# Optimization experiments

Hardware: AMD Instinct MI355X
Metric: run time of the kernel (lower is better)

Reference implementation:

```python
import jax, jax.numpy as jnp
import numpy as np

N, S, SKV, K, V = 16, 4096, 4096, 64, 64


def setup_inputs() -> dict:
    key = jax.random.key(0)
    k1, k2, k3, k4 = jax.random.split(key, 4)
    return {
        "queries": jax.random.normal(k1, (N, S, K), dtype=jnp.float32),
        "keys": jax.random.normal(k2, (N, SKV, K), dtype=jnp.float32),
        "values": jax.random.normal(k3, (N, SKV, V), dtype=jnp.float32),
        "mask": jax.random.normal(k4, (S, SKV), dtype=jnp.float32),
    }


def reference(queries, keys, values, mask):
    # queries scaled by K^{-1/2}, then baddbmm(mask, q, k^T)
    scale = queries.shape[-1] ** -0.5
    q = queries * scale
    # scores: [N, S, SKV]; mask (S, SKV) broadcasts over batch like baddbmm
    scores = jnp.einsum('nsk,ntk->nst', q, keys) + mask
    attn_weights = jax.nn.softmax(scores, axis=-1)
    # attn: [N, S, V]; dropout_p = 0.0 (eval), needs_weights = False
    attn = jnp.einsum('nst,ntv->nsv', attn_weights, values)
    return attn
```

## Files before the change

### kernel.cpp

```cpp
#include <hip/hip_runtime.h>
#include <cstdint>
#include <cstddef>


typedef __attribute__((ext_vector_type(8))) short short8;
typedef __attribute__((ext_vector_type(4))) short short4v;
typedef __attribute__((ext_vector_type(4))) float f32x4;
typedef __attribute__((ext_vector_type(4))) unsigned int uint4v;
typedef __attribute__((ext_vector_type(2))) unsigned int uint2v;

#define DEV __device__ __forceinline__

constexpr int N_B   = 16;
constexpr int S_Q   = 4096;
constexpr int S_KV  = 4096;
constexpr int DH    = 64;
constexpr int BQ    = 128;
constexpr int BK    = 64;
constexpr int ITERS = S_KV / BK;
constexpr int KSTR  = 72;
constexpr int VSTR  = 68;

#define LOG2E 1.44269504088896340736f
#define QSCALE (0.125f * 1.44269504088896340736f)

DEV unsigned short f2bf(float f) {
  union { float f; unsigned int i; } x; x.f = f;
  unsigned int r = x.i + 0x7FFFu + ((x.i >> 16) & 1u);
  return (unsigned short)(r >> 16);
}

#if __has_builtin(__builtin_amdgcn_cvt_pk_bf16_f32)
typedef __attribute__((ext_vector_type(2))) __bf16 bf16x2v;
DEV unsigned int packrne(float a, float b) {
  union { bf16x2v v; unsigned int u; } x;
  x.v = __builtin_amdgcn_cvt_pk_bf16_f32(a, b);
  return x.u;
}
#else
DEV unsigned int packrne(float a, float b) {
  union { float f; unsigned int u; } ua, ub; ua.f = a; ub.f = b;
  unsigned int ra = ua.u + 0x7FFFu + ((ua.u >> 16) & 1u);
  unsigned int rb = ub.u + 0x7FFFu + ((ub.u >> 16) & 1u);
  return __builtin_amdgcn_perm(rb, ra, 0x07060302u);
}
#endif

DEV f32x4 mfma16(short4v a, short4v b, f32x4 c) {
#if __has_builtin(__builtin_amdgcn_mfma_f32_16x16x16bf16_1k)
  return __builtin_amdgcn_mfma_f32_16x16x16bf16_1k(a, b, c, 0, 0, 0);
#elif __has_builtin(__builtin_amdgcn_mfma_f32_16x16x16_bf16)
  return __builtin_amdgcn_mfma_f32_16x16x16_bf16(a, b, c, 0, 0, 0);
#else
  asm volatile("v_mfma_f32_16x16x16_bf16 %0, %1, %2, %0\n\ts_nop 7\n\ts_nop 7"
               : "+v"(c) : "v"(a), "v"(b));
  return c;
#endif
}

DEV void stageK(unsigned short* buf, const f32x4* L, int tS) {
  const int r0 = tS >> 3, c = tS & 7;
  uint4v d0, d1;
  d0[0] = packrne(L[0][0], L[0][1]); d0[1] = packrne(L[0][2], L[0][3]);
  d0[2] = packrne(L[1][0], L[1][1]); d0[3] = packrne(L[1][2], L[1][3]);
  d1[0] = packrne(L[2][0], L[2][1]); d1[1] = packrne(L[2][2], L[2][3]);
  d1[2] = packrne(L[3][0], L[3][1]); d1[3] = packrne(L[3][2], L[3][3]);
  *(uint4v*)&buf[r0 * KSTR + c * 8]        = d0;
  *(uint4v*)&buf[(r0 + 32) * KSTR + c * 8] = d1;
}

DEV void stageV(unsigned short* buf, const f32x4* L, int tS) {
  const int a = tS >> 4;
  const int x = tS & 15;
  const int slot = (a + x) & 15;
#pragma unroll
  for (int j = 0; j < 4; ++j) {
    uint2v d;
    d[0] = packrne(L[0][j], L[1][j]);
    d[1] = packrne(L[2][j], L[3][j]);
    *(uint2v*)&buf[(x * 4 + j) * VSTR + slot * 4] = d;
  }
}

template <int MW>
__global__ __launch_bounds__(512, MW)
void sdpa_fwd(const float* __restrict__ Qg,
              const float* __restrict__ Kg,
              const float* __restrict__ Vg,
              const float* __restrict__ Mg,
              float* __restrict__ Ob,
              float* __restrict__ Lb,
              int nIter)
{
  __shared__ __align__(16) unsigned short ldsK[2][BK * KSTR];
  __shared__ __align__(16) unsigned short ldsV[2][DH * VSTR];

  const int n    = blockIdx.y;
  const int q0   = blockIdx.x * BQ;
  const int z    = blockIdx.z;
  const size_t kvbase = (size_t)z * (size_t)nIter * BK;
  const int t    = threadIdx.x;
  const int w    = t >> 6;
  const int lane = t & 63;
  const int l15  = lane & 15;
  const int quad = lane >> 4;
  const int qrow = q0 + w * 16 + l15;

  short8 qf0, qf1;
  {
    const float* qp = Qg + ((size_t)n * S_Q + (size_t)qrow) * DH + quad * 8;
#pragma unroll
    for (int j = 0; j < 8; ++j) {
      qf0[j] = (short)f2bf(qp[j] * QSCALE);
      qf1[j] = (short)f2bf(qp[32 + j] * QSCALE);
    }
  }

  const bool isK = (w < 4);
  const int  tS  = t & 255;
  const float* sgp =
      isK ? Kg + ((size_t)n * S_KV + kvbase + (size_t)(tS >> 3)) * DH
              + (tS & 7) * 8
          : Vg + ((size_t)n * S_KV + kvbase + (size_t)(tS >> 4) * 4) * DH
              + (tS & 15) * 4;

  const float* mrow = Mg + (size_t)qrow * S_KV + kvbase + quad * 4;

  f32x4 acc[4];
#pragma unroll
  for (int nt = 0; nt < 4; ++nt)
#pragma unroll
    for (int r = 0; r < 4; ++r) acc[nt][r] = 0.0f;

  float rs = 0.0f;

  {
    f32x4 L[4];
    if (isK) {
      L[0] = *(const f32x4*)(sgp);
      L[1] = *(const f32x4*)(sgp + 4);
      L[2] = *(const f32x4*)(sgp + 32 * DH);
      L[3] = *(const f32x4*)(sgp + 32 * DH + 4);
      stageK(&ldsK[0][0], L, tS);
    } else {
#pragma unroll
      for (int i = 0; i < 4; ++i) L[i] = *(const f32x4*)(sgp + i * DH);
      stageV(&ldsV[0][0], L, tS);
    }
  }
  __syncthreads();

  for (int it = 0; it < nIter; ++it) {
    const int p   = it & 1;
    const int kv0 = it * BK;
    const bool more = (it + 1 < nIter);

    short4v pf[4];
#pragma unroll
    for (int h = 0; h < 4; ++h) {
      const short8 kf0 =
          *(const short8*)&ldsK[p][(l15 + 16 * h) * KSTR + quad * 8];
      const short8 kf1 =
          *(const short8*)&ldsK[p][(l15 + 16 * h) * KSTR + (quad + 4) * 8];
      const f32x4 mk = *(const f32x4*)(mrow + kv0 + 16 * h);
      f32x4 c = {0.f, 0.f, 0.f, 0.f};
      __builtin_amdgcn_s_setprio(1);
      c = __builtin_amdgcn_mfma_f32_16x16x32_bf16(kf0, qf0, c, 0, 0, 0);
      c = __builtin_amdgcn_mfma_f32_16x16x32_bf16(kf1, qf1, c, 0, 0, 0);
      __builtin_amdgcn_s_setprio(0);
      float e[4];
#pragma unroll
      for (int r = 0; r < 4; ++r)
        e[r] = __builtin_amdgcn_exp2f(fmaf(mk[r], LOG2E, c[r]));
      rs += (e[0] + e[1]) + (e[2] + e[3]);
      union { uint2v u; short4v s; } ue;
      ue.u[0] = packrne(e[0], e[1]);
      ue.u[1] = packrne(e[2], e[3]);
      pf[h] = ue.s;
    }

    f32x4 L[4];
    if (more) {
      const float* np = sgp + (size_t)(kv0 + BK) * DH;
      if (isK) {
        L[0] = *(const f32x4*)(np);
        L[1] = *(const f32x4*)(np + 4);
        L[2] = *(const f32x4*)(np + 32 * DH);
        L[3] = *(const f32x4*)(np + 32 * DH + 4);
      } else {
#pragma unroll
        for (int i = 0; i < 4; ++i) L[i] = *(const f32x4*)(np + i * DH);
      }
    }

    __builtin_amdgcn_s_setprio(1);
#pragma unroll
    for (int nt = 0; nt < 4; ++nt) {
      const int vcol = l15 + 16 * nt;
      const int xr   = (l15 >> 2) + 4 * nt;
#pragma unroll
      for (int h = 0; h < 4; ++h) {
        const int slot = ((4 * h + quad) + xr) & 15;
        short4v vf = *(const short4v*)&ldsV[p][vcol * VSTR + slot * 4];
        acc[nt] = mfma16(vf, pf[h], acc[nt]);
      }
    }
    __builtin_amdgcn_s_setprio(0);

    if (more) {
      if (isK) stageK(&ldsK[p ^ 1][0], L, tS);
      else     stageV(&ldsV[p ^ 1][0], L, tS);
    }
    __syncthreads();
  }

  rs += __shfl_xor(rs, 16, 64);
  rs += __shfl_xor(rs, 32, 64);

  if (Lb) {
    const size_t NSV = (size_t)N_B * S_Q * DH;
    float* ob = Ob + (size_t)z * NSV + ((size_t)n * S_Q + (size_t)qrow) * DH
              + quad * 4;
#pragma unroll
    for (int nt = 0; nt < 4; ++nt) *(f32x4*)(ob + 16 * nt) = acc[nt];
    if (quad == 0) {
      float* lp = Lb + (size_t)z * ((size_t)N_B * S_Q) + (size_t)n * S_Q
                + (size_t)qrow;
      lp[0] = rs;
    }
  } else {
    const float inv = 1.0f / rs;
    float* ob = Ob + ((size_t)n * S_Q + (size_t)qrow) * DH + quad * 4;
#pragma unroll
    for (int nt = 0; nt < 4; ++nt) {
      f32x4 o;
#pragma unroll
      for (int r = 0; r < 4; ++r) o[r] = acc[nt][r] * inv;
      *(f32x4*)(ob + 16 * nt) = o;
    }
  }
}

__global__ __launch_bounds__(256)
void sdpa_combine(const float* __restrict__ ws, float* __restrict__ Og) {
  constexpr size_t NSV = (size_t)N_B * S_Q * DH;
  constexpr size_t NS  = (size_t)N_B * S_Q;
  const size_t i = (size_t)blockIdx.x * 256 + threadIdx.x;
  const f32x4* A0 = (const f32x4*)ws;
  const f32x4* A1 = A0 + NSV / 4;
  const float* L0 = ws + 2 * NSV;
  const float* L1 = L0 + NS;
  const size_t qi = i >> 4;
  const f32x4 a = A0[i], b = A1[i];
  const float inv = 1.0f / (L0[qi] + L1[qi]);
  f32x4 o;
#pragma unroll
  for (int r = 0; r < 4; ++r) o[r] = (a[r] + b[r]) * inv;
  ((f32x4*)Og)[i] = o;
}

extern "C" void kernel_launch(void* const* d_in, const int* in_sizes, int n_in,
                              void* d_out, int out_size, void* d_ws, size_t ws_size,
                              hipStream_t stream) {
  (void)in_sizes; (void)n_in; (void)out_size;
  const float* q = (const float*)d_in[0];
  const float* k = (const float*)d_in[1];
  const float* v = (const float*)d_in[2];
  const float* m = (const float*)d_in[3];
  float* o = (float*)d_out;

  constexpr size_t NSV = (size_t)N_B * S_Q * DH;
  constexpr size_t NS  = (size_t)N_B * S_Q;
  constexpr size_t WS_NEED = (2 * NSV + 2 * NS) * sizeof(float);

  static int use8 = -1;
  if (use8 < 0) {
    hipFuncAttributes attr{};
    use8 = 0;
    if (hipFuncGetAttributes(&attr,
            reinterpret_cast<const void*>(&sdpa_fwd<8>)) == hipSuccess &&
        attr.localSizeBytes == 0)
      use8 = 1;
  }

  if (use8 && d_ws != nullptr && ws_size >= WS_NEED) {
    float* ws = (float*)d_ws;
    dim3 grid(S_Q / BQ, N_B, 2);
    hipLaunchKernelGGL(sdpa_fwd<8>, grid, dim3(512), 0, stream,
                       q, k, v, m, ws, ws + 2 * NSV, ITERS / 2);
    hipLaunchKernelGGL(sdpa_combine, dim3((unsigned)(NSV / 4 / 256)), dim3(256),
                       0, stream, (const float*)ws, o);
  } else {
    dim3 grid(S_Q / BQ, N_B, 1);
    hipLaunchKernelGGL(sdpa_fwd<4>, grid, dim3(512), 0, stream,
                       q, k, v, m, o, (float*)nullptr, ITERS);
  }
}
```

Before: 307.9 us.

## Pre-convert K/V tiles to bf16 LDS images and DMA them directly into LDS

Adds a prep kernel that converts each 64-row K and V tile to bf16 in the exact padded, swizzled LDS layout and writes it to workspace. The main kernel then copies these images straight into LDS with global_load_lds, issued before the QK step, so it no longer does per-iteration fp32 register loads, conversion and LDS stores. This halves the K/V bytes read by the main loop and frees VALU and registers. In exchange it adds an extra kernel launch and an extra pass over K/V, and it requires more workspace.

```diff
diff --git a/kernel.cpp b/kernel.cpp
--- a/kernel.cpp
+++ b/kernel.cpp
@@ -20,6 +20,9 @@
 constexpr int ITERS = S_KV / BK;
 constexpr int KSTR  = 72;
 constexpr int VSTR  = 68;
+constexpr int KIMG_B = 9216;
+constexpr int VIMG_B = 9216;
+constexpr int TILE_B = KIMG_B + VIMG_B;
 
 #define LOG2E 1.44269504088896340736f
 #define QSCALE (0.125f * 1.44269504088896340736f)
@@ -82,29 +85,82 @@
   }
 }
 
+DEV void dma16(const void* g, void* l) {
+#if __has_builtin(__builtin_amdgcn_global_load_lds)
+  __builtin_amdgcn_global_load_lds(
+      (const __attribute__((address_space(1))) unsigned int*)g,
+      (__attribute__((address_space(3))) unsigned int*)l, 16, 0, 0);
+#else
+  ((uint4v*)l)[threadIdx.x & 63] = *(const uint4v*)g;
+#endif
+}
+
+DEV void dmaTile(const char* gt, void* lk, void* lv, int w, int laneB) {
+  if (w < 4) {
+    const int base = w * 2048;
+    dma16(gt + base + laneB,        (char*)lk + base);
+    dma16(gt + base + 1024 + laneB, (char*)lk + base + 1024);
+    if (w == 0) dma16(gt + 8192 + laneB, (char*)lk + 8192);
+  } else {
+    const char* g = gt + KIMG_B;
+    const int base = (w - 4) * 2048;
+    dma16(g + base + laneB,        (char*)lv + base);
+    dma16(g + base + 1024 + laneB, (char*)lv + base + 1024);
+    if (w == 4) dma16(g + 8192 + laneB, (char*)lv + 8192);
+  }
+}
+
+__global__ __launch_bounds__(256)
+void sdpa_prep(const float* __restrict__ Kg, const float* __restrict__ Vg,
+               unsigned short* __restrict__ imgs) {
+  const int b   = blockIdx.x;
+  const int n   = b >> 6, tau = b & 63;
+  const int tS  = threadIdx.x;
+  unsigned short* img = imgs + (size_t)b * (TILE_B / 2);
+  {
+    const float* kp =
+        Kg + ((size_t)n * S_KV + tau * 64 + (tS >> 3)) * DH + (tS & 7) * 8;
+    f32x4 L[4];
+    L[0] = *(const f32x4*)(kp);
+    L[1] = *(const f32x4*)(kp + 4);
+    L[2] = *(const f32x4*)(kp + 32 * DH);
+    L[3] = *(const f32x4*)(kp + 32 * DH + 4);
+    stageK(img, L, tS);
+  }
+  {
+    const float* vp =
+        Vg + ((size_t)n * S_KV + tau * 64 + (size_t)(tS >> 4) * 4) * DH
+           + (tS & 15) * 4;
+    f32x4 L[4];
+#pragma unroll
+    for (int i = 0; i < 4; ++i) L[i] = *(const f32x4*)(vp + i * DH);
+    stageV(img + KIMG_B / 2, L, tS);
+  }
+}
+
 template <int MW>
 __global__ __launch_bounds__(512, MW)
-void sdpa_fwd(const float* __restrict__ Qg,
-              const float* __restrict__ Kg,
-              const float* __restrict__ Vg,
-              const float* __restrict__ Mg,
-              float* __restrict__ Ob,
-              float* __restrict__ Lb,
-              int nIter)
+void sdpa_fwd_dma(const float* __restrict__ Qg,
+                  const float* __restrict__ Mg,
+                  const unsigned short* __restrict__ imgs,
+                  float* __restrict__ Ob,
+                  float* __restrict__ Lb,
+                  int nIter)
 {
-  __shared__ __align__(16) unsigned short ldsK[2][BK * KSTR];
-  __shared__ __align__(16) unsigned short ldsV[2][DH * VSTR];
-
-  const int n    = blockIdx.y;
-  const int q0   = blockIdx.x * BQ;
-  const int z    = blockIdx.z;
-  const size_t kvbase = (size_t)z * (size_t)nIter * BK;
-  const int t    = threadIdx.x;
-  const int w    = t >> 6;
-  const int lane = t & 63;
-  const int l15  = lane & 15;
-  const int quad = lane >> 4;
-  const int qrow = q0 + w * 16 + l15;
+  __shared__ __align__(16) unsigned short ldsK[2][KIMG_B / 2];
+  __shared__ __align__(16) unsigned short ldsV[2][VIMG_B / 2];
+
+  const int n     = blockIdx.y;
+  const int q0    = blockIdx.x * BQ;
+  const int z     = blockIdx.z;
+  const int t     = threadIdx.x;
+  const int w     = t >> 6;
+  const int lane  = t & 63;
+  const int l15   = lane & 15;
+  const int quad  = lane >> 4;
+  const int qrow  = q0 + w * 16 + l15;
+  const int laneB = lane * 16;
+  const int tbase = n * 64 + z * nIter;
 
   short8 qf0, qf1;
   {
@@ -116,44 +172,28 @@
     }
   }
 
-  const bool isK = (w < 4);
-  const int  tS  = t & 255;
-  const float* sgp =
-      isK ? Kg + ((size_t)n * S_KV + kvbase + (size_t)(tS >> 3)) * DH
-              + (tS & 7) * 8
-          : Vg + ((size_t)n * S_KV + kvbase + (size_t)(tS >> 4) * 4) * DH
-              + (tS & 15) * 4;
-
-  const float* mrow = Mg + (size_t)qrow * S_KV + kvbase + quad * 4;
+  const float* mrow =
+      Mg + (size_t)qrow * S_KV + (size_t)z * nIter * BK + quad * 4;
 
   f32x4 acc[4];
 #pragma unroll
   for (int nt = 0; nt < 4; ++nt)
 #pragma unroll
     for (int r = 0; r < 4; ++r) acc[nt][r] = 0.0f;
-
   float rs = 0.0f;
 
-  {
-    f32x4 L[4];
-    if (isK) {
-      L[0] = *(const f32x4*)(sgp);
-      L[1] = *(const f32x4*)(sgp + 4);
-      L[2] = *(const f32x4*)(sgp + 32 * DH);
-      L[3] = *(const f32x4*)(sgp + 32 * DH + 4);
-      stageK(&ldsK[0][0], L, tS);
-    } else {
-#pragma unroll
-      for (int i = 0; i < 4; ++i) L[i] = *(const f32x4*)(sgp + i * DH);
-      stageV(&ldsV[0][0], L, tS);
-    }
-  }
+  dmaTile((const char*)imgs + (size_t)tbase * TILE_B,
+          &ldsK[0][0], &ldsV[0][0], w, laneB);
   __syncthreads();
 
   for (int it = 0; it < nIter; ++it) {
     const int p   = it & 1;
     const int kv0 = it * BK;
     const bool more = (it + 1 < nIter);
+
+    if (more)
+      dmaTile((const char*)imgs + (size_t)(tbase + it + 1) * TILE_B,
+              &ldsK[p ^ 1][0], &ldsV[p ^ 1][0], w, laneB);
 
     short4v pf[4];
 #pragma unroll
@@ -179,6 +219,125 @@
       pf[h] = ue.s;
     }
 
+    __builtin_amdgcn_s_setprio(1);
+#pragma unroll
+    for (int nt = 0; nt < 4; ++nt) {
+      const int vcol = l15 + 16 * nt;
+      const int xr   = (l15 >> 2) + 4 * nt;
+#pragma unroll
+      for (int h = 0; h < 4; ++h) {
+        const int slot = ((4 * h + quad) + xr) & 15;
+        short4v vf = *(const short4v*)&ldsV[p][vcol * VSTR + slot * 4];
+        acc[nt] = mfma16(vf, pf[h], acc[nt]);
+      }
+    }
+    __builtin_amdgcn_s_setprio(0);
+
+    __syncthreads();
+  }
+
+  rs += __shfl_xor(rs, 16, 64);
+  rs += __shfl_xor(rs, 32, 64);
+
+  if (Lb) {
+    const size_t NSV = (size_t)N_B * S_Q * DH;
+    float* ob = Ob + (size_t)z * NSV + ((size_t)n * S_Q + (size_t)qrow) * DH
+              + quad * 4;
+#pragma unroll
+    for (int nt = 0; nt < 4; ++nt) *(f32x4*)(ob + 16 * nt) = acc[nt];
+    if (quad == 0) {
+      float* lp = Lb + (size_t)z * ((size_t)N_B * S_Q) + (size_t)n * S_Q
+                + (size_t)qrow;
+      lp[0] = rs;
+    }
+  } else {
+    const float inv = 1.0f / rs;
+    float* ob = Ob + ((size_t)n * S_Q + (size_t)qrow) * DH + quad * 4;
+#pragma unroll
+    for (int nt = 0; nt < 4; ++nt) {
+      f32x4 o;
+#pragma unroll
+      for (int r = 0; r < 4; ++r) o[r] = acc[nt][r] * inv;
+      *(f32x4*)(ob + 16 * nt) = o;
+    }
+  }
+}
+
+__global__ __launch_bounds__(512, 4)
+void sdpa_fwd_reg(const float* __restrict__ Qg, const float* __restrict__ Kg,
+                  const float* __restrict__ Vg, const float* __restrict__ Mg,
+                  float* __restrict__ Og)
+{
+  __shared__ __align__(16) unsigned short ldsK[2][BK * KSTR];
+  __shared__ __align__(16) unsigned short ldsV[2][DH * VSTR];
+
+  const int n = blockIdx.y, q0 = blockIdx.x * BQ, t = threadIdx.x;
+  const int w = t >> 6, lane = t & 63, l15 = lane & 15, quad = lane >> 4;
+  const int qrow = q0 + w * 16 + l15;
+
+  short8 qf0, qf1;
+  {
+    const float* qp = Qg + ((size_t)n * S_Q + (size_t)qrow) * DH + quad * 8;
+#pragma unroll
+    for (int j = 0; j < 8; ++j) {
+      qf0[j] = (short)f2bf(qp[j] * QSCALE);
+      qf1[j] = (short)f2bf(qp[32 + j] * QSCALE);
+    }
+  }
+  const bool isK = (w < 4);
+  const int  tS  = t & 255;
+  const float* sgp =
+      isK ? Kg + ((size_t)n * S_KV + (size_t)(tS >> 3)) * DH + (tS & 7) * 8
+          : Vg + ((size_t)n * S_KV + (size_t)(tS >> 4) * 4) * DH + (tS & 15) * 4;
+  const float* mrow = Mg + (size_t)qrow * S_KV + quad * 4;
+
+  f32x4 acc[4];
+#pragma unroll
+  for (int nt = 0; nt < 4; ++nt)
+#pragma unroll
+    for (int r = 0; r < 4; ++r) acc[nt][r] = 0.0f;
+  float rs = 0.0f;
+
+  {
+    f32x4 L[4];
+    if (isK) {
+      L[0] = *(const f32x4*)(sgp);
+      L[1] = *(const f32x4*)(sgp + 4);
+      L[2] = *(const f32x4*)(sgp + 32 * DH);
+      L[3] = *(const f32x4*)(sgp + 32 * DH + 4);
+      stageK(&ldsK[0][0], L, tS);
+    } else {
+#pragma unroll
+      for (int i = 0; i < 4; ++i) L[i] = *(const f32x4*)(sgp + i * DH);
+      stageV(&ldsV[0][0], L, tS);
+    }
+  }
+  __syncthreads();
+
+  for (int it = 0; it < ITERS; ++it) {
+    const int p = it & 1, kv0 = it * BK;
+    const bool more = (it + 1 < ITERS);
+    short4v pf[4];
+#pragma unroll
+    for (int h = 0; h < 4; ++h) {
+      const short8 kf0 =
+          *(const short8*)&ldsK[p][(l15 + 16 * h) * KSTR + quad * 8];
+      const short8 kf1 =
+          *(const short8*)&ldsK[p][(l15 + 16 * h) * KSTR + (quad + 4) * 8];
+      const f32x4 mk = *(const f32x4*)(mrow + kv0 + 16 * h);
+      f32x4 c = {0.f, 0.f, 0.f, 0.f};
+      c = __builtin_amdgcn_mfma_f32_16x16x32_bf16(kf0, qf0, c, 0, 0, 0);
+      c = __builtin_amdgcn_mfma_f32_16x16x32_bf16(kf1, qf1, c, 0, 0, 0);
+      float e[4];
+#pragma unroll
+      for (int r = 0; r < 4; ++r)
+        e[r] = __builtin_amdgcn_exp2f(fmaf(mk[r], LOG2E, c[r]));
+      rs += (e[0] + e[1]) + (e[2] + e[3]);
+      union { uint2v u; short4v s; } ue;
+      ue.u[0] = packrne(e[0], e[1]);
+      ue.u[1] = packrne(e[2], e[3]);
+      pf[h] = ue.s;
+    }
     f32x4 L[4];
     if (more) {
       const float* np = sgp + (size_t)(kv0 + BK) * DH;
@@ -192,8 +351,6 @@
         for (int i = 0; i < 4; ++i) L[i] = *(const f32x4*)(np + i * DH);
       }
     }
-
-    __builtin_amdgcn_s_setprio(1);
 #pragma unroll
     for (int nt = 0; nt < 4; ++nt) {
       const int vcol = l15 + 16 * nt;
@@ -205,8 +362,6 @@
         acc[nt] = mfma16(vf, pf[h], acc[nt]);
       }
     }
-    __builtin_amdgcn_s_setprio(0);
-
     if (more) {
       if (isK) stageK(&ldsK[p ^ 1][0], L, tS);
       else     stageV(&ldsV[p ^ 1][0], L, tS);
@@ -216,28 +371,14 @@
 
   rs += __shfl_xor(rs, 16, 64);
   rs += __shfl_xor(rs, 32, 64);
-
-  if (Lb) {
-    const size_t NSV = (size_t)N_B * S_Q * DH;
-    float* ob = Ob + (size_t)z * NSV + ((size_t)n * S_Q + (size_t)qrow) * DH
-              + quad * 4;
-#pragma unroll
-    for (int nt = 0; nt < 4; ++nt) *(f32x4*)(ob + 16 * nt) = acc[nt];
-    if (quad == 0) {
-      float* lp = Lb + (size_t)z * ((size_t)N_B * S_Q) + (size_t)n * S_Q
-                + (size_t)qrow;
-      lp[0] = rs;
-    }
-  } else {
-    const float inv = 1.0f / rs;
-    float* ob = Ob + ((size_t)n * S_Q + (size_t)qrow) * DH + quad * 4;
-#pragma unroll
-    for (int nt = 0; nt < 4; ++nt) {
-      f32x4 o;
-#pragma unroll
-      for (int r = 0; r < 4; ++r) o[r] = acc[nt][r] * inv;
-      *(f32x4*)(ob + 16 * nt) = o;
-    }
+  const float inv = 1.0f / rs;
+  float* ob = Og + ((size_t)n * S_Q + (size_t)qrow) * DH + quad * 4;
+#pragma unroll
+  for (int nt = 0; nt < 4; ++nt) {
+    f32x4 o;
+#pragma unroll
+    for (int r = 0; r < 4; ++r) o[r] = acc[nt][r] * inv;
+    *(f32x4*)(ob + 16 * nt) = o;
   }
 }
 
@@ -271,28 +412,39 @@
 
   constexpr size_t NSV = (size_t)N_B * S_Q * DH;
   constexpr size_t NS  = (size_t)N_B * S_Q;
-  constexpr size_t WS_NEED = (2 * NSV + 2 * NS) * sizeof(float);
+  constexpr size_t IMG_BYTES = (size_t)N_B * 64 * TILE_B;
+  constexpr size_t SPL_BYTES = (2 * NSV + 2 * NS) * sizeof(float);
 
   static int use8 = -1;
   if (use8 < 0) {
     hipFuncAttributes attr{};
     use8 = 0;
     if (hipFuncGetAttributes(&attr,
-            reinterpret_cast<const void*>(&sdpa_fwd<8>)) == hipSuccess &&
+            reinterpret_cast<const void*>(&sdpa_fwd_dma<8>)) == hipSuccess &&
         attr.localSizeBytes == 0)
       use8 = 1;
   }
 
-  if (use8 && d_ws != nullptr && ws_size >= WS_NEED) {
-    float* ws = (float*)d_ws;
+  if (d_ws != nullptr && ws_size >= IMG_BYTES + SPL_BYTES && use8) {
+    unsigned short* imgs = (unsigned short*)d_ws;
+    float* part = (float*)((char*)d_ws + IMG_BYTES);
+    hipLaunchKernelGGL(sdpa_prep, dim3(N_B * 64), dim3(256), 0, stream,
+                       k, v, imgs);
     dim3 grid(S_Q / BQ, N_B, 2);
-    hipLaunchKernelGGL(sdpa_fwd<8>, grid, dim3(512), 0, stream,
-                       q, k, v, m, ws, ws + 2 * NSV, ITERS / 2);
-    hipLaunchKernelGGL(sdpa_combine, dim3((unsigned)(NSV / 4 / 256)), dim3(256),
-                       0, stream, (const float*)ws, o);
+    hipLaunchKernelGGL((sdpa_fwd_dma<8>), grid, dim3(512), 0, stream,
+                       q, m, imgs, part, part + 2 * NSV, ITERS / 2);
+    hipLaunchKernelGGL(sdpa_combine, dim3((unsigned)(NSV / 4 / 256)),
+                       dim3(256), 0, stream, (const float*)part, o);
+  } else if (d_ws != nullptr && ws_size >= IMG_BYTES) {
+    unsigned short* imgs = (unsigned short*)d_ws;
+    hipLaunchKernelGGL(sdpa_prep, dim3(N_B * 64), dim3(256), 0, stream,
+                       k, v, imgs);
+    dim3 grid(S_Q / BQ, N_B, 1);
+    hipLaunchKernelGGL((sdpa_fwd_dma<4>), grid, dim3(512), 0, stream,
+                       q, m, imgs, o, (float*)nullptr, ITERS);
   } else {
-    dim3 grid(S_Q / BQ, N_B, 1);
-    hipLaunchKernelGGL(sdpa_fwd<4>, grid, dim3(512), 0, stream,
-                       q, k, v, m, o, (float*)nullptr, ITERS);
-  }
-}
+    dim3 grid(S_Q / BQ, N_B);
+    hipLaunchKernelGGL(sdpa_fwd_reg, grid, dim3(512), 0, stream,
+                       q, k, v, m, o);
+  }
+}
```

After: 295.7 us. 3.9% less time.
